# Optimization experiments

Measured on AMD Instinct MI355X. Metric: run time of the kernel, lower is better.

The kernel has to match this reference:

```python
import jax, jax.numpy as jnp
import numpy as np

B, N, D, H = 256, 40, 256, 256      # molecules, atoms/molecule, pc_hidden, pred_hidden
nS, nC, nB = 40, 5, 5               # n_SYMBOLS, n_FORMAL_CHARGES, n_BOND_TYPES
NEG_SLOPE = 0.01                    # F.leaky_relu default


def _lrelu(x):
    return jnp.where(x >= 0, x, NEG_SLOPE * x)


def setup_inputs() -> dict:
    key = jax.random.key(0)
    ks = jax.random.split(key, 7)
    def w(k, shape, fan_in):
        return jax.random.normal(k, shape, jnp.float32) / np.float32(np.sqrt(fan_in))
    return {
        "yhat": jax.random.normal(ks[0], (B, N, D), jnp.float32),
        "Ws1": w(ks[1], (D, H), D),      "bs1": jnp.zeros((H,), jnp.float32),
        "Ws2": w(ks[2], (H, nS), H),     "bs2": jnp.zeros((nS,), jnp.float32),
        "Wc1": w(ks[3], (D, H), D),      "bc1": jnp.zeros((H,), jnp.float32),
        "Wc2": w(ks[4], (H, nC), H),     "bc2": jnp.zeros((nC,), jnp.float32),
        "Wb1": w(ks[5], (2 * D, H), 2 * D), "bb1": jnp.zeros((H,), jnp.float32),
        "Wb2": w(ks[6], (H, nB), H),     "bb2": jnp.zeros((nB,), jnp.float32),
    }


def reference(yhat, Ws1, bs1, Ws2, bs2, Wc1, bc1, Wc2, bc2, Wb1, bb1, Wb2, bb2):
    # Per-atom symbol / charge heads (2-layer MLP with leaky_relu)
    symbols = _lrelu(yhat @ Ws1 + bs1) @ Ws2 + bs2          # [B, N, nS]
    charges = _lrelu(yhat @ Wc1 + bc1) @ Wc2 + bc2          # [B, N, nC]

    # Pairwise bond head: concat(x_i, x_j) @ Wb1 == x_i @ Wb1[:D] + x_j @ Wb1[D:]
    # (avoids materializing the [B, N, N, 2D] concat tensor)
    p1 = yhat @ Wb1[:D]                                      # [B, N, H]
    p2 = yhat @ Wb1[D:]                                      # [B, N, H]
    h = _lrelu(p1[:, :, None, :] + p2[:, None, :, :] + bb1)  # [B, N, N, H]
    bonds = h @ Wb2 + bb2                                    # [B, N, N, nB]
    bonds = bonds + jnp.swapaxes(bonds, 1, 2)                # symmetrize (i,j)+(j,i)

    return (symbols.reshape(-1, nS),
            charges.reshape(-1, nC),
            bonds.reshape(-1, nB))
```

## Files before the change

kernel.cpp:

```cpp
#include <hip/hip_runtime.h>
#include <hip/hip_bf16.h>

typedef unsigned short u16;
typedef __attribute__((ext_vector_type(4))) int   int4v;
typedef __attribute__((ext_vector_type(4))) unsigned int uint4v;
typedef __attribute__((ext_vector_type(4))) unsigned short ushort4v;
typedef __attribute__((ext_vector_type(4))) float floatx4;
typedef __attribute__((ext_vector_type(8))) short bf16x8;

#define LRELU_NS 0.01f
#define SK 264

__device__ __forceinline__ float bitsToF(unsigned int b) {
    union { unsigned int u; float f; } v; v.u = b << 16; return v.f;
}
__device__ __forceinline__ float bfLo(unsigned int d) {
    union { unsigned int u; float f; } v; v.u = d << 16; return v.f;
}
__device__ __forceinline__ float bfHi(unsigned int d) {
    union { unsigned int u; float f; } v; v.u = d & 0xffff0000u; return v.f;
}
__device__ __forceinline__ u16 f2bf(float f) {
    __hip_bfloat16 h = __float2bfloat16(f);
    return *reinterpret_cast<u16*>(&h);
}
__device__ __forceinline__ float lrelu(float v) {
    return fmaxf(v, 0.f) + LRELU_NS * fminf(v, 0.f);
}
__device__ __forceinline__ u16 ldW(const void* p, int i, int isF32) {
    return isF32 ? f2bf(((const float*)p)[i]) : ((const u16*)p)[i];
}
__device__ __forceinline__ float ldF(const void* p, int i, int isF32) {
    return isF32 ? ((const float*)p)[i]
                 : bitsToF((unsigned int)((const u16*)p)[i]);
}

__device__ __forceinline__ int computeIsF32(const u16* y, int* cnt, int t) {
    if (t == 0) *cnt = 0;
    __syncthreads();
    if (t < 256) {
        u16 v = y[2 * t];
        int e = (v >> 7) & 0xFF;
        if (v == 0 || (e >= 96 && e < 160)) atomicAdd(cnt, 1);
    }
    __syncthreads();
    return (*cnt < 192) ? 1 : 0;
}

__global__ __launch_bounds__(256) void pack_kernel(
    const void* __restrict__ yhat,
    const void* __restrict__ Ws1, const void* __restrict__ Wc1,
    const void* __restrict__ Wb1, const void* __restrict__ Ws2,
    const void* __restrict__ Wc2,
    const void* __restrict__ bs1, const void* __restrict__ bc1,
    const void* __restrict__ bb1, const void* __restrict__ bs2,
    const void* __restrict__ bc2, const void* __restrict__ bb2,
    u16* __restrict__ WallT, u16* __restrict__ W2T, float* __restrict__ biasF)
{
    __shared__ int fcnt;
    const int bid = blockIdx.x, t = threadIdx.x;
    const int isF32 = computeIsF32((const u16*)yhat, &fcnt, t);
    if (bid < 64) {
        __shared__ u16 tile[64][65];
        const int c0 = (bid & 15) * 64;
        const int k0 = (bid >> 4) * 64;
        const void* src; int coff; int roff = 0;
        if (c0 < 256)      { src = Ws1; coff = c0; }
        else if (c0 < 512) { src = Wc1; coff = c0 - 256; }
        else if (c0 < 768) { src = Wb1; coff = c0 - 512; }
        else               { src = Wb1; coff = c0 - 768; roff = 256; }
        const int cc = t & 63, kk0 = t >> 6;
        #pragma unroll
        for (int i = 0; i < 16; ++i) {
            int kk = kk0 + i * 4;
            tile[kk][cc] = ldW(src, (k0 + kk + roff) * 256 + coff + cc, isF32);
        }
        __syncthreads();
        const int kk2 = t & 63, cc0 = t >> 6;
        #pragma unroll
        for (int i = 0; i < 16; ++i) {
            int cc2 = cc0 + i * 4;
            WallT[(c0 + cc2) * 256 + (k0 + kk2)] = tile[kk2][cc2];
        }
    } else if (bid < 128) {
        int e2 = (bid - 64) * 256 + t;
        int c = e2 >> 8, k = e2 & 255;
        u16 v = 0;
        if (c < 40)                 v = ldW(Ws2, k * 40 + c, isF32);
        else if (c >= 48 && c < 53) v = ldW(Wc2, k * 5 + (c - 48), isF32);
        W2T[c * 256 + k] = v;
    } else {
        int idx = (bid - 128) * 256 + t;
        float v = 0.f;
        if (idx < 256)       v = ldF(bs1, idx, isF32);
        else if (idx < 512)  v = ldF(bc1, idx - 256, isF32);
        else if (idx < 768)  v = ldF(bb1, idx - 512, isF32);
        else if (idx < 808)  v = ldF(bs2, idx - 768, isF32);
        else if (idx < 813)  v = ldF(bc2, idx - 808, isF32);
        else if (idx >= 816 && idx < 821) v = ldF(bb2, idx - 816, isF32);
        biasF[idx] = v;
    }
}

__global__ __launch_bounds__(256) void heads_kernel(
    const void* __restrict__ Xv, const u16* __restrict__ WallT,
    const u16* __restrict__ W2T, const float* __restrict__ biasF,
    void* __restrict__ outv)
{
    __shared__ u16 Xs[64 * SK];
    __shared__ u16 Hb[64 * SK];
    __shared__ int fcnt;
    const int t = threadIdx.x;
    const int bm0 = blockIdx.x * 64;
    const int head = blockIdx.y;
    const int isF32 = computeIsF32((const u16*)Xv, &fcnt, t);

    if (isF32) {
        const floatx4* __restrict__ src = (const floatx4*)((const float*)Xv + bm0 * 256);
        #pragma unroll
        for (int it = 0; it < 16; ++it) {
            int cid = t + it * 256;
            int row = cid >> 6, ch = cid & 63;
            floatx4 f = src[cid];
            ushort4v u;
            u[0] = f2bf(f[0]); u[1] = f2bf(f[1]); u[2] = f2bf(f[2]); u[3] = f2bf(f[3]);
            *(ushort4v*)&Xs[row * SK + ch * 4] = u;
        }
    } else {
        const int4v* __restrict__ src = (const int4v*)((const u16*)Xv + bm0 * 256);
        #pragma unroll
        for (int it = 0; it < 8; ++it) {
            int cid = t + it * 256;
            int row = cid >> 5, ch = cid & 31;
            *(int4v*)&Xs[row * SK + ch * 8] = src[cid];
        }
    }
    __syncthreads();

    const int w = t >> 6, l = t & 63;
    const int ml = l & 15, kq = l >> 4, r0 = kq * 4;

    for (int n = 0; n < 4; ++n) {
        const int ct = w + 4 * n;
        floatx4 acc[4] = {};
        #pragma unroll
        for (int ks = 0; ks < 8; ++ks) {
            const int k0 = ks * 32 + kq * 8;
            bf16x8 bf = *(const bf16x8*)&WallT[(head * 256 + ct * 16 + ml) * 256 + k0];
            #pragma unroll
            for (int mt = 0; mt < 4; ++mt) {
                bf16x8 a = *(const bf16x8*)&Xs[(mt * 16 + ml) * SK + k0];
                acc[mt] = __builtin_amdgcn_mfma_f32_16x16x32_bf16(a, bf, acc[mt], 0, 0, 0);
            }
        }
        const int col = ct * 16 + ml;
        const float bias = biasF[head * 256 + col];
        #pragma unroll
        for (int mt = 0; mt < 4; ++mt)
            #pragma unroll
            for (int r = 0; r < 4; ++r)
                Hb[(mt * 16 + r0 + r) * SK + col] = f2bf(lrelu(acc[mt][r] + bias));
    }
    __syncthreads();

    const int nct = (head == 0) ? 3 : 1;
    const int c0  = (head == 0) ? 0 : 48;
    floatx4 acc2[3] = {};
    #pragma unroll
    for (int ks = 0; ks < 8; ++ks) {
        const int k0 = ks * 32 + kq * 8;
        bf16x8 a = *(const bf16x8*)&Hb[(w * 16 + ml) * SK + k0];
        #pragma unroll
        for (int j = 0; j < 3; ++j) {
            if (j < nct) {
                bf16x8 bf = *(const bf16x8*)&W2T[(c0 + j * 16 + ml) * 256 + k0];
                acc2[j] = __builtin_amdgcn_mfma_f32_16x16x32_bf16(a, bf, acc2[j], 0, 0, 0);
            }
        }
    }
    #pragma unroll
    for (int j = 0; j < 3; ++j) {
        if (j < nct) {
            const int col = j * 16 + ml;
            const int lim = (head == 0) ? 40 : 5;
            if (col < lim) {
                const float bias = biasF[(head == 0 ? 768 : 808) + col];
                #pragma unroll
                for (int r = 0; r < 4; ++r) {
                    const int row = bm0 + w * 16 + r0 + r;
                    const int o = (head == 0) ? row * 40 + col
                                              : 409600 + row * 5 + col;
                    const float v = acc2[j][r] + bias;
                    if (isF32) ((float*)outv)[o] = v;
                    else ((__hip_bfloat16*)outv)[o] = __float2bfloat16(v);
                }
            }
        }
    }
}

__global__ __launch_bounds__(512) void bonds_kernel(
    const void* __restrict__ Xv, const u16* __restrict__ WallT,
    const void* __restrict__ Wb2, const float* __restrict__ biasF,
    void* __restrict__ outv)
{
    __shared__ u16 Xm[48 * SK];
    __shared__ u16 P1L[48 * SK];
    __shared__ u16 P2L[48 * SK];
    __shared__ u16 WsB[16 * 264];
    __shared__ float fbuf[8000];
    __shared__ int fcnt;
    const int t = threadIdx.x, b = blockIdx.x;
    const int isF32 = computeIsF32((const u16*)Xv, &fcnt, t);

    if (isF32) {
        const floatx4* __restrict__ src = (const floatx4*)((const float*)Xv + b * 10240);
        #pragma unroll
        for (int it = 0; it < 5; ++it) {
            int cid = t + it * 512;
            int row = cid >> 6, ch = cid & 63;
            floatx4 f = src[cid];
            ushort4v u;
            u[0] = f2bf(f[0]); u[1] = f2bf(f[1]); u[2] = f2bf(f[2]); u[3] = f2bf(f[3]);
            *(ushort4v*)&Xm[row * SK + ch * 4] = u;
        }
        {
            int row = 40 + (t >> 6), ch = t & 63;
            ushort4v z = {0, 0, 0, 0};
            *(ushort4v*)&Xm[row * SK + ch * 4] = z;
        }
    } else {
        const int4v* __restrict__ src = (const int4v*)((const u16*)Xv + b * 10240);
        #pragma unroll
        for (int it = 0; it < 3; ++it) {
            int cid = t + it * 512;
            int row = cid >> 5, ch = cid & 31;
            if (cid < 1280) *(int4v*)&Xm[row * SK + ch * 8] = src[cid];
            else { int4v z = {0, 0, 0, 0}; *(int4v*)&Xm[row * SK + ch * 8] = z; }
        }
    }
    #pragma unroll
    for (int it = 0; it < 8; ++it) {
        int e2 = t + it * 512;
        int c = e2 >> 8, k = e2 & 255;
        WsB[c * 264 + k] = (c < 5) ? ldW(Wb2, k * 5 + c, isF32) : (u16)0;
    }
    __syncthreads();

    const int w = t >> 6, l = t & 63;
    const int ml = l & 15, kq = l >> 4, r0 = kq * 4;

    for (int n = 0; n < 4; ++n) {
        const int gc = (w + 8 * n) * 16 + ml;
        floatx4 acc[3] = {};
        #pragma unroll
        for (int ks = 0; ks < 8; ++ks) {
            const int k0 = ks * 32 + kq * 8;
            bf16x8 bf = *(const bf16x8*)&WallT[(512 + gc) * 256 + k0];
            #pragma unroll
            for (int i = 0; i < 3; ++i) {
                bf16x8 a = *(const bf16x8*)&Xm[(i * 16 + ml) * SK + k0];
                acc[i] = __builtin_amdgcn_mfma_f32_16x16x32_bf16(a, bf, acc[i], 0, 0, 0);
            }
        }
        u16* dst = (gc < 256) ? P1L : P2L;
        const int col = gc & 255;
        const float bias = (gc < 256) ? biasF[512 + gc] : 0.f;
        #pragma unroll
        for (int i = 0; i < 3; ++i)
            #pragma unroll
            for (int r = 0; r < 4; ++r)
                dst[(i * 16 + r0 + r) * SK + col] = f2bf(acc[i][r] + bias);
    }
    __syncthreads();

    bf16x8 wf[8];
    #pragma unroll
    for (int ks = 0; ks < 8; ++ks)
        wf[ks] = *(const bf16x8*)&WsB[ml * 264 + ks * 32 + kq * 8];

    for (int m = 0; m < 5; ++m) {
        const int i = w + 8 * m;
        uint4v pa8[8];
        #pragma unroll
        for (int ks = 0; ks < 8; ++ks)
            pa8[ks] = *(const uint4v*)&P1L[i * SK + ks * 32 + kq * 8];
        for (int jt = 0; jt < 3; ++jt) {
            floatx4 acc = {};
            #pragma unroll
            for (int ks = 0; ks < 8; ++ks) {
                const int k0 = ks * 32 + kq * 8;
                uint4v pa = pa8[ks];
                uint4v pb = *(const uint4v*)&P2L[(jt * 16 + ml) * SK + k0];
                bf16x8 af;
                #pragma unroll
                for (int d = 0; d < 4; ++d) {
                    af[2 * d]     = (short)f2bf(lrelu(bfLo(pa[d]) + bfLo(pb[d])));
                    af[2 * d + 1] = (short)f2bf(lrelu(bfHi(pa[d]) + bfHi(pb[d])));
                }
                acc = __builtin_amdgcn_mfma_f32_16x16x32_bf16(af, wf[ks], acc, 0, 0, 0);
            }
            if (ml < 5) {
                #pragma unroll
                for (int r = 0; r < 4; ++r) {
                    const int j = jt * 16 + r0 + r;
                    if (j < 40) fbuf[(i * 40 + j) * 5 + ml] = acc[r];
                }
            }
        }
    }
    __syncthreads();

    const int base = 460800 + b * 8000;
    for (int e = t; e < 8000; e += 512) {
        int pr = e / 5, c = e - pr * 5;
        int i = pr / 40, j = pr - (pr / 40) * 40;
        float v = fbuf[e] + fbuf[(j * 40 + i) * 5 + c] + 2.f * biasF[816 + c];
        if (isF32) ((float*)outv)[base + e] = v;
        else ((__hip_bfloat16*)outv)[base + e] = __float2bfloat16(v);
    }
}

extern "C" void kernel_launch(void* const* d_in, const int* in_sizes, int n_in,
                              void* d_out, int out_size, void* d_ws, size_t ws_size,
                              hipStream_t stream)
{
    const void* yhat = d_in[0];
    const void* Ws1  = d_in[1];
    const void* bs1  = d_in[2];
    const void* Ws2  = d_in[3];
    const void* bs2  = d_in[4];
    const void* Wc1  = d_in[5];
    const void* bc1  = d_in[6];
    const void* Wc2  = d_in[7];
    const void* bc2  = d_in[8];
    const void* Wb1  = d_in[9];
    const void* bb1  = d_in[10];
    const void* Wb2  = d_in[11];
    const void* bb2  = d_in[12];

    char* wsb = (char*)d_ws;
    float* biasF = (float*)(wsb + 4096);
    u16*   W2T   = (u16*)(wsb + 8192);
    u16*   WallT = (u16*)(wsb + 40960);

    pack_kernel<<<132, 256, 0, stream>>>(yhat, Ws1, Wc1, Wb1, Ws2, Wc2,
                                         bs1, bc1, bb1, bs2, bc2, bb2,
                                         WallT, W2T, biasF);
    heads_kernel<<<dim3(160, 2), 256, 0, stream>>>(yhat, WallT, W2T, biasF, d_out);
    bonds_kernel<<<256, 512, 0, stream>>>(yhat, WallT, Wb2, biasF, d_out);
}
```

Baseline: 139.1 us.

## Split bond head into projection and symmetric pair kernels with folded symmetrization

```diff
diff --git a/kernel.cpp b/kernel.cpp
--- a/kernel.cpp
+++ b/kernel.cpp
@@ -25,7 +25,7 @@
     return *reinterpret_cast<u16*>(&h);
 }
 __device__ __forceinline__ float lrelu(float v) {
-    return fmaxf(v, 0.f) + LRELU_NS * fminf(v, 0.f);
+    return fmaxf(v, LRELU_NS * v);
 }
 __device__ __forceinline__ u16 ldW(const void* p, int i, int isF32) {
     return isF32 ? f2bf(((const float*)p)[i]) : ((const u16*)p)[i];
@@ -199,6 +199,152 @@
     }
 }
 
+__global__ __launch_bounds__(512) void l1p_kernel(
+    const void* __restrict__ Xv, const u16* __restrict__ WallT,
+    const float* __restrict__ biasF,
+    u16* __restrict__ P1g, u16* __restrict__ P2g)
+{
+    __shared__ u16 Xs[64 * SK];
+    __shared__ int fcnt;
+    const int t = threadIdx.x;
+    const int bm0 = blockIdx.x * 64;
+    const int isF32 = computeIsF32((const u16*)Xv, &fcnt, t);
+
+    if (isF32) {
+        const floatx4* __restrict__ src = (const floatx4*)((const float*)Xv + bm0 * 256);
+        #pragma unroll
+        for (int s = 0; s < 8; ++s) {
+            int cid = t + s * 512;
+            int row = cid >> 6, ch = cid & 63;
+            floatx4 f = src[cid];
+            ushort4v u;
+            u[0] = f2bf(f[0]); u[1] = f2bf(f[1]); u[2] = f2bf(f[2]); u[3] = f2bf(f[3]);
+            *(ushort4v*)&Xs[row * SK + ch * 4] = u;
+        }
+    } else {
+        const int4v* __restrict__ src = (const int4v*)((const u16*)Xv + bm0 * 256);
+        #pragma unroll
+        for (int s = 0; s < 4; ++s) {
+            int cid = t + s * 512;
+            int row = cid >> 5, ch = cid & 31;
+            *(int4v*)&Xs[row * SK + ch * 8] = src[cid];
+        }
+    }
+    __syncthreads();
+
+    const int w = t >> 6, l = t & 63;
+    const int ml = l & 15, kq = l >> 4, r0 = kq * 4;
+    const int ct = blockIdx.y * 8 + w;
+    const int gc = ct * 16 + ml;
+
+    floatx4 acc[4] = {};
+    #pragma unroll
+    for (int ks = 0; ks < 8; ++ks) {
+        const int k0 = ks * 32 + kq * 8;
+        bf16x8 bf = *(const bf16x8*)&WallT[(512 + gc) * 256 + k0];
+        #pragma unroll
+        for (int mt = 0; mt < 4; ++mt) {
+            bf16x8 a = *(const bf16x8*)&Xs[(mt * 16 + ml) * SK + k0];
+            acc[mt] = __builtin_amdgcn_mfma_f32_16x16x32_bf16(a, bf, acc[mt], 0, 0, 0);
+        }
+    }
+    const float bias = (gc < 256) ? biasF[512 + gc] : 0.f;
+    u16* __restrict__ dst = (gc < 256) ? P1g : P2g;
+    const int col = gc & 255;
+    #pragma unroll
+    for (int mt = 0; mt < 4; ++mt)
+        #pragma unroll
+        for (int r = 0; r < 4; ++r)
+            dst[(bm0 + mt * 16 + r0 + r) * 256 + col] = f2bf(acc[mt][r] + bias);
+}
+
+__global__ __launch_bounds__(512, 4) void pairf_kernel(
+    const void* __restrict__ Xv,
+    const u16* __restrict__ P1g, const u16* __restrict__ P2g,
+    const void* __restrict__ Wb2, const float* __restrict__ biasF,
+    void* __restrict__ outv)
+{
+    __shared__ u16 Pq[4][16 * SK];
+    __shared__ u16 WsB[16 * 264];
+    __shared__ int fcnt;
+    const int t = threadIdx.x, mol = blockIdx.x;
+    const int y = blockIdx.y;
+    const int it = (y < 3) ? 0 : (y < 5) ? 1 : 2;
+    const int jt = (y < 3) ? y : (y < 5) ? (y - 2) : 2;
+    const int isF32 = computeIsF32((const u16*)Xv, &fcnt, t);
+
+    #pragma unroll
+    for (int s = 0; s < 4; ++s) {
+        const int cid = t + s * 512;
+        const int buf = cid >> 9, r = (cid >> 5) & 15, ch = cid & 31;
+        const int tile = (buf < 2) ? it : jt;
+        const u16* __restrict__ src = (buf & 1) ? P2g : P1g;
+        const int arow = tile * 16 + r;
+        int4v v = {0, 0, 0, 0};
+        if (arow < 40) v = *(const int4v*)&src[(mol * 40 + arow) * 256 + ch * 8];
+        *(int4v*)&Pq[buf][r * SK + ch * 8] = v;
+    }
+    #pragma unroll
+    for (int s = 0; s < 8; ++s) {
+        const int e2 = t + s * 512;
+        const int c = e2 >> 8, k = e2 & 255;
+        WsB[c * 264 + k] = (c < 5) ? ldW(Wb2, k * 5 + c, isF32) : (u16)0;
+    }
+    __syncthreads();
+
+    const int w = t >> 6, l = t & 63;
+    const int ml = l & 15, kq = l >> 4, r0 = kq * 4;
+
+    bf16x8 wf[8];
+    #pragma unroll
+    for (int ks = 0; ks < 8; ++ks)
+        wf[ks] = *(const bf16x8*)&WsB[ml * 264 + ks * 32 + kq * 8];
+    const float b2x2 = 2.f * biasF[816 + ml];
+
+    for (int ii = 0; ii < 2; ++ii) {
+        const int iloc = w + 8 * ii;
+        const int i = it * 16 + iloc;
+        if (i >= 40) continue;
+        floatx4 acc = {};
+        #pragma unroll
+        for (int ks = 0; ks < 8; ++ks) {
+            const int k0 = ks * 32 + kq * 8;
+            uint4v a1 = *(const uint4v*)&Pq[0][iloc * SK + k0];
+            uint4v a2 = *(const uint4v*)&Pq[1][iloc * SK + k0];
+            uint4v b1 = *(const uint4v*)&Pq[2][ml * SK + k0];
+            uint4v b2 = *(const uint4v*)&Pq[3][ml * SK + k0];
+            bf16x8 af;
+            #pragma unroll
+            for (int d = 0; d < 4; ++d) {
+                const float sLo = lrelu(bfLo(a1[d]) + bfLo(b2[d]))
+                                + lrelu(bfLo(b1[d]) + bfLo(a2[d]));
+                const float sHi = lrelu(bfHi(a1[d]) + bfHi(b2[d]))
+                                + lrelu(bfHi(b1[d]) + bfHi(a2[d]));
+                af[2 * d]     = (short)f2bf(sLo);
+                af[2 * d + 1] = (short)f2bf(sHi);
+            }
+            acc = __builtin_amdgcn_mfma_f32_16x16x32_bf16(af, wf[ks], acc, 0, 0, 0);
+        }
+        if (ml < 5) {
+            #pragma unroll
+            for (int r = 0; r < 4; ++r) {
+                const int j = jt * 16 + r0 + r;
+                if (j < 40 && (it != jt || j >= i)) {
+                    const float v = acc[r] + b2x2;
+                    const int o1 = 460800 + (mol * 1600 + i * 40 + j) * 5 + ml;
+                    if (isF32) ((float*)outv)[o1] = v;
+                    else ((__hip_bfloat16*)outv)[o1] = __float2bfloat16(v);
+                    if (it != jt || j > i) {
+                        const int o2 = 460800 + (mol * 1600 + j * 40 + i) * 5 + ml;
+                        if (isF32) ((float*)outv)[o2] = v;
+                        else ((__hip_bfloat16*)outv)[o2] = __float2bfloat16(v);
+                    }
+                }
+            }
+        }
+    }
+}
+
 __global__ __launch_bounds__(512) void bonds_kernel(
     const void* __restrict__ Xv, const u16* __restrict__ WallT,
     const void* __restrict__ Wb2, const float* __restrict__ biasF,
@@ -343,10 +489,20 @@
     float* biasF = (float*)(wsb + 4096);
     u16*   W2T   = (u16*)(wsb + 8192);
     u16*   WallT = (u16*)(wsb + 40960);
+    const size_t P_OFF   = 565248;
+    const size_t P_BYTES = (size_t)10240 * 256 * 2;
+    const bool big = ws_size >= P_OFF + 2 * P_BYTES;
 
     pack_kernel<<<132, 256, 0, stream>>>(yhat, Ws1, Wc1, Wb1, Ws2, Wc2,
                                          bs1, bc1, bb1, bs2, bc2, bb2,
                                          WallT, W2T, biasF);
     heads_kernel<<<dim3(160, 2), 256, 0, stream>>>(yhat, WallT, W2T, biasF, d_out);
-    bonds_kernel<<<256, 512, 0, stream>>>(yhat, WallT, Wb2, biasF, d_out);
-}
+    if (big) {
+        u16* P1g = (u16*)(wsb + P_OFF);
+        u16* P2g = (u16*)(wsb + P_OFF + P_BYTES);
+        l1p_kernel<<<dim3(160, 4), 512, 0, stream>>>(yhat, WallT, biasF, P1g, P2g);
+        pairf_kernel<<<dim3(256, 6), 512, 0, stream>>>(yhat, P1g, P2g, Wb2, biasF, d_out);
+    } else {
+        bonds_kernel<<<256, 512, 0, stream>>>(yhat, WallT, Wb2, biasF, d_out);
+    }
+}
```

Result: slower. 146.5 us (+5.3%).

## Compute only upper-triangle bond tiles, symmetrize in registers, widen heads blocks

Applied to the files above, without the earlier changes.

```diff
diff --git a/kernel.cpp b/kernel.cpp
--- a/kernel.cpp
+++ b/kernel.cpp
@@ -25,7 +25,7 @@
     return *reinterpret_cast<u16*>(&h);
 }
 __device__ __forceinline__ float lrelu(float v) {
-    return fmaxf(v, 0.f) + LRELU_NS * fminf(v, 0.f);
+    return fmaxf(v, LRELU_NS * v);
 }
 __device__ __forceinline__ u16 ldW(const void* p, int i, int isF32) {
     return isF32 ? f2bf(((const float*)p)[i]) : ((const u16*)p)[i];
@@ -102,7 +102,7 @@
     }
 }
 
-__global__ __launch_bounds__(256) void heads_kernel(
+__global__ __launch_bounds__(512) void heads2_kernel(
     const void* __restrict__ Xv, const u16* __restrict__ WallT,
     const u16* __restrict__ W2T, const float* __restrict__ biasF,
     void* __restrict__ outv)
@@ -118,8 +118,8 @@
     if (isF32) {
         const floatx4* __restrict__ src = (const floatx4*)((const float*)Xv + bm0 * 256);
         #pragma unroll
-        for (int it = 0; it < 16; ++it) {
-            int cid = t + it * 256;
+        for (int s = 0; s < 8; ++s) {
+            int cid = t + s * 512;
             int row = cid >> 6, ch = cid & 63;
             floatx4 f = src[cid];
             ushort4v u;
@@ -129,8 +129,8 @@
     } else {
         const int4v* __restrict__ src = (const int4v*)((const u16*)Xv + bm0 * 256);
         #pragma unroll
-        for (int it = 0; it < 8; ++it) {
-            int cid = t + it * 256;
+        for (int s = 0; s < 4; ++s) {
+            int cid = t + s * 512;
             int row = cid >> 5, ch = cid & 31;
             *(int4v*)&Xs[row * SK + ch * 8] = src[cid];
         }
@@ -140,8 +140,9 @@
     const int w = t >> 6, l = t & 63;
     const int ml = l & 15, kq = l >> 4, r0 = kq * 4;
 
-    for (int n = 0; n < 4; ++n) {
-        const int ct = w + 4 * n;
+    #pragma unroll
+    for (int n = 0; n < 2; ++n) {
+        const int ct = w + 8 * n;
         floatx4 acc[4] = {};
         #pragma unroll
         for (int ks = 0; ks < 8; ++ks) {
@@ -163,43 +164,45 @@
     }
     __syncthreads();
 
-    const int nct = (head == 0) ? 3 : 1;
-    const int c0  = (head == 0) ? 0 : 48;
-    floatx4 acc2[3] = {};
-    #pragma unroll
-    for (int ks = 0; ks < 8; ++ks) {
-        const int k0 = ks * 32 + kq * 8;
-        bf16x8 a = *(const bf16x8*)&Hb[(w * 16 + ml) * SK + k0];
+    if (w < 4) {
+        const int nct = (head == 0) ? 3 : 1;
+        const int c0  = (head == 0) ? 0 : 48;
+        floatx4 acc2[3] = {};
+        #pragma unroll
+        for (int ks = 0; ks < 8; ++ks) {
+            const int k0 = ks * 32 + kq * 8;
+            bf16x8 a = *(const bf16x8*)&Hb[(w * 16 + ml) * SK + k0];
+            #pragma unroll
+            for (int j = 0; j < 3; ++j) {
+                if (j < nct) {
+                    bf16x8 bf = *(const bf16x8*)&W2T[(c0 + j * 16 + ml) * 256 + k0];
+                    acc2[j] = __builtin_amdgcn_mfma_f32_16x16x32_bf16(a, bf, acc2[j], 0, 0, 0);
+                }
+            }
+        }
         #pragma unroll
         for (int j = 0; j < 3; ++j) {
             if (j < nct) {
-                bf16x8 bf = *(const bf16x8*)&W2T[(c0 + j * 16 + ml) * 256 + k0];
-                acc2[j] = __builtin_amdgcn_mfma_f32_16x16x32_bf16(a, bf, acc2[j], 0, 0, 0);
-            }
-        }
-    }
-    #pragma unroll
-    for (int j = 0; j < 3; ++j) {
-        if (j < nct) {
-            const int col = j * 16 + ml;
-            const int lim = (head == 0) ? 40 : 5;
-            if (col < lim) {
-                const float bias = biasF[(head == 0 ? 768 : 808) + col];
-                #pragma unroll
-                for (int r = 0; r < 4; ++r) {
-                    const int row = bm0 + w * 16 + r0 + r;
-                    const int o = (head == 0) ? row * 40 + col
-                                              : 409600 + row * 5 + col;
-                    const float v = acc2[j][r] + bias;
-                    if (isF32) ((float*)outv)[o] = v;
-                    else ((__hip_bfloat16*)outv)[o] = __float2bfloat16(v);
+                const int col = j * 16 + ml;
+                const int lim = (head == 0) ? 40 : 5;
+                if (col < lim) {
+                    const float bias = biasF[(head == 0 ? 768 : 808) + col];
+                    #pragma unroll
+                    for (int r = 0; r < 4; ++r) {
+                        const int row = bm0 + w * 16 + r0 + r;
+                        const int o = (head == 0) ? row * 40 + col
+                                                  : 409600 + row * 5 + col;
+                        const float v = acc2[j][r] + bias;
+                        if (isF32) ((float*)outv)[o] = v;
+                        else ((__hip_bfloat16*)outv)[o] = __float2bfloat16(v);
+                    }
                 }
             }
         }
     }
 }
 
-__global__ __launch_bounds__(512) void bonds_kernel(
+__global__ __launch_bounds__(512) void bonds2_kernel(
     const void* __restrict__ Xv, const u16* __restrict__ WallT,
     const void* __restrict__ Wb2, const float* __restrict__ biasF,
     void* __restrict__ outv)
@@ -207,8 +210,7 @@
     __shared__ u16 Xm[48 * SK];
     __shared__ u16 P1L[48 * SK];
     __shared__ u16 P2L[48 * SK];
-    __shared__ u16 WsB[16 * 264];
-    __shared__ float fbuf[8000];
+    __shared__ u16 WsB[5 * 264];
     __shared__ int fcnt;
     const int t = threadIdx.x, b = blockIdx.x;
     const int isF32 = computeIsF32((const u16*)Xv, &fcnt, t);
@@ -216,8 +218,8 @@
     if (isF32) {
         const floatx4* __restrict__ src = (const floatx4*)((const float*)Xv + b * 10240);
         #pragma unroll
-        for (int it = 0; it < 5; ++it) {
-            int cid = t + it * 512;
+        for (int s = 0; s < 5; ++s) {
+            int cid = t + s * 512;
             int row = cid >> 6, ch = cid & 63;
             floatx4 f = src[cid];
             ushort4v u;
@@ -232,18 +234,20 @@
     } else {
         const int4v* __restrict__ src = (const int4v*)((const u16*)Xv + b * 10240);
         #pragma unroll
-        for (int it = 0; it < 3; ++it) {
-            int cid = t + it * 512;
+        for (int s = 0; s < 3; ++s) {
+            int cid = t + s * 512;
             int row = cid >> 5, ch = cid & 31;
             if (cid < 1280) *(int4v*)&Xm[row * SK + ch * 8] = src[cid];
             else { int4v z = {0, 0, 0, 0}; *(int4v*)&Xm[row * SK + ch * 8] = z; }
         }
     }
     #pragma unroll
-    for (int it = 0; it < 8; ++it) {
-        int e2 = t + it * 512;
-        int c = e2 >> 8, k = e2 & 255;
-        WsB[c * 264 + k] = (c < 5) ? ldW(Wb2, k * 5 + c, isF32) : (u16)0;
+    for (int s = 0; s < 3; ++s) {
+        int e2 = t + s * 512;
+        if (e2 < 1280) {
+            int c = e2 >> 8, k = e2 & 255;
+            WsB[c * 264 + k] = ldW(Wb2, k * 5 + c, isF32);
+        }
     }
     __syncthreads();
 
@@ -274,50 +278,55 @@
     }
     __syncthreads();
 
+    const int sel = (ml < 5) ? ml : 4;
     bf16x8 wf[8];
     #pragma unroll
     for (int ks = 0; ks < 8; ++ks)
-        wf[ks] = *(const bf16x8*)&WsB[ml * 264 + ks * 32 + kq * 8];
+        wf[ks] = *(const bf16x8*)&WsB[sel * 264 + ks * 32 + kq * 8];
+    const float b2x2 = 2.f * biasF[816 + ml];
 
     for (int m = 0; m < 5; ++m) {
         const int i = w + 8 * m;
-        uint4v pa8[8];
-        #pragma unroll
-        for (int ks = 0; ks < 8; ++ks)
-            pa8[ks] = *(const uint4v*)&P1L[i * SK + ks * 32 + kq * 8];
-        for (int jt = 0; jt < 3; ++jt) {
-            floatx4 acc = {};
+        const int itile = i >> 4;
+        for (int jt = itile; jt < 3; ++jt) {
+            floatx4 accF = {}, accB = {};
             #pragma unroll
             for (int ks = 0; ks < 8; ++ks) {
                 const int k0 = ks * 32 + kq * 8;
-                uint4v pa = pa8[ks];
-                uint4v pb = *(const uint4v*)&P2L[(jt * 16 + ml) * SK + k0];
-                bf16x8 af;
+                const uint4v a1 = *(const uint4v*)&P1L[i * SK + k0];
+                const uint4v a2 = *(const uint4v*)&P2L[i * SK + k0];
+                const uint4v b1 = *(const uint4v*)&P1L[(jt * 16 + ml) * SK + k0];
+                const uint4v b2 = *(const uint4v*)&P2L[(jt * 16 + ml) * SK + k0];
+                bf16x8 afF, afB;
                 #pragma unroll
                 for (int d = 0; d < 4; ++d) {
-                    af[2 * d]     = (short)f2bf(lrelu(bfLo(pa[d]) + bfLo(pb[d])));
-                    af[2 * d + 1] = (short)f2bf(lrelu(bfHi(pa[d]) + bfHi(pb[d])));
+                    afF[2 * d]     = (short)f2bf(lrelu(bfLo(a1[d]) + bfLo(b2[d])));
+                    afF[2 * d + 1] = (short)f2bf(lrelu(bfHi(a1[d]) + bfHi(b2[d])));
+                    afB[2 * d]     = (short)f2bf(lrelu(bfLo(b1[d]) + bfLo(a2[d])));
+                    afB[2 * d + 1] = (short)f2bf(lrelu(bfHi(b1[d]) + bfHi(a2[d])));
                 }
-                acc = __builtin_amdgcn_mfma_f32_16x16x32_bf16(af, wf[ks], acc, 0, 0, 0);
+                accF = __builtin_amdgcn_mfma_f32_16x16x32_bf16(afF, wf[ks], accF, 0, 0, 0);
+                accB = __builtin_amdgcn_mfma_f32_16x16x32_bf16(afB, wf[ks], accB, 0, 0, 0);
             }
             if (ml < 5) {
+                const bool diag = (jt == itile);
                 #pragma unroll
                 for (int r = 0; r < 4; ++r) {
                     const int j = jt * 16 + r0 + r;
-                    if (j < 40) fbuf[(i * 40 + j) * 5 + ml] = acc[r];
+                    if (j < 40 && (!diag || j >= i)) {
+                        const float v = accF[r] + accB[r] + b2x2;
+                        const int o1 = 460800 + (b * 1600 + i * 40 + j) * 5 + ml;
+                        if (isF32) ((float*)outv)[o1] = v;
+                        else ((__hip_bfloat16*)outv)[o1] = __float2bfloat16(v);
+                        if (!diag || j > i) {
+                            const int o2 = 460800 + (b * 1600 + j * 40 + i) * 5 + ml;
+                            if (isF32) ((float*)outv)[o2] = v;
+                            else ((__hip_bfloat16*)outv)[o2] = __float2bfloat16(v);
+                        }
+                    }
                 }
             }
         }
-    }
-    __syncthreads();
-
-    const int base = 460800 + b * 8000;
-    for (int e = t; e < 8000; e += 512) {
-        int pr = e / 5, c = e - pr * 5;
-        int i = pr / 40, j = pr - (pr / 40) * 40;
-        float v = fbuf[e] + fbuf[(j * 40 + i) * 5 + c] + 2.f * biasF[816 + c];
-        if (isF32) ((float*)outv)[base + e] = v;
-        else ((__hip_bfloat16*)outv)[base + e] = __float2bfloat16(v);
     }
 }
 
@@ -347,6 +356,6 @@
     pack_kernel<<<132, 256, 0, stream>>>(yhat, Ws1, Wc1, Wb1, Ws2, Wc2,
                                          bs1, bc1, bb1, bs2, bc2, bb2,
                                          WallT, W2T, biasF);
-    heads_kernel<<<dim3(160, 2), 256, 0, stream>>>(yhat, WallT, W2T, biasF, d_out);
-    bonds_kernel<<<256, 512, 0, stream>>>(yhat, WallT, Wb2, biasF, d_out);
-}
+    heads2_kernel<<<dim3(160, 2), 512, 0, stream>>>(yhat, WallT, W2T, biasF, d_out);
+    bonds2_kernel<<<256, 512, 0, stream>>>(yhat, WallT, Wb2, biasF, d_out);
+}
```

After: 146.5 us. +5.3%, slower.
